# Kernel tuning notes

Measured on AMD Instinct MI355X. Metric: run time of the kernel, lower is better.

The kernel has to match this reference:

```python
import jax, jax.numpy as jnp
import numpy as np

B, C, W, H = 4, 256, 64, 64
DK = C // 8  # query/key channels


def setup_inputs() -> dict:
    key = jax.random.key(0)
    ks = jax.random.split(key, 7)
    x = jax.random.normal(ks[0], (B, C, W, H), dtype=jnp.float32)
    # conv1x1 weights stored as [out_ch, in_ch]
    Wq = jax.random.normal(ks[1], (DK, C), dtype=jnp.float32) / np.sqrt(C)
    bq = jnp.zeros((DK,), dtype=jnp.float32)
    Wk = jax.random.normal(ks[2], (DK, C), dtype=jnp.float32) / np.sqrt(C)
    bk = jnp.zeros((DK,), dtype=jnp.float32)
    Wv = jax.random.normal(ks[3], (C, C), dtype=jnp.float32) / np.sqrt(C)
    bv = jnp.zeros((C,), dtype=jnp.float32)
    gamma = jnp.zeros((1,), dtype=jnp.float32)
    return {"x": x, "Wq": Wq, "bq": bq, "Wk": Wk, "bk": bk,
            "Wv": Wv, "bv": bv, "gamma": gamma}


def reference(x, Wq, bq, Wk, bk, Wv, bv, gamma):
    b, c, w, h = x.shape
    n = w * h
    xf = x.reshape(b, c, n)                     # [B, C, N]
    # conv1x1 == channel matmul
    q = jnp.einsum('dc,bcn->bnd', Wq, xf) + bq  # [B, N, DK]
    k = jnp.einsum('dc,bcn->bdn', Wk, xf) + bk[None, :, None]  # [B, DK, N]
    energy = jnp.einsum('bnd,bdm->bnm', q, k)   # [B, N, N]
    attention = jax.nn.softmax(energy, axis=-1)
    v = jnp.einsum('dc,bcn->bdn', Wv, xf) + bv[None, :, None]  # [B, C, N]
    out = jnp.einsum('bdm,bnm->bdn', v, attention)              # [B, C, N]
    out = out.reshape(b, c, w, h)
    out = gamma * out + x
    return out, attention
```

## Files before the change

### kernel.cpp

```cpp
#include <hip/hip_runtime.h>
#include <hip/hip_bf16.h>

typedef __attribute__((ext_vector_type(8))) short bf16x8;
typedef __attribute__((ext_vector_type(4))) float f32x4;
typedef __attribute__((ext_vector_type(4))) unsigned int u32x4;
typedef __attribute__((ext_vector_type(2))) unsigned int u32x2;

#define B_SZ 4
#define C_SZ 256
#define N_SZ 4096
#define DK_SZ 32

#define WQB_OFF 0
#define WKB_OFF 8192
#define WVB_OFF 16384
#define QB_OFF  81920
#define KB_OFF  606208
#define VB_OFF  1130496

__device__ __forceinline__ short f2bf(float f) {
    union { float f; unsigned int u; } v; v.f = f;
    unsigned int r = v.u + 0x7fffu + ((v.u >> 16) & 1u);
    return (short)(r >> 16);
}

__device__ __forceinline__ unsigned int cvt_pk_bf16(float lo, float hi) {
    unsigned int r;
    asm volatile("v_cvt_pk_bf16_f32 %0, %1, %2" : "=v"(r) : "v"(lo), "v"(hi));
    return r;
}

__device__ __forceinline__ f32x4 mfma16(bf16x8 a, bf16x8 b, f32x4 c) {
    return __builtin_amdgcn_mfma_f32_16x16x32_bf16(a, b, c, 0, 0, 0);
}

__device__ __forceinline__ void gload_lds16(const void* g, void* l) {
    __builtin_amdgcn_global_load_lds((const __attribute__((address_space(1))) unsigned int*)g,
                                     (__attribute__((address_space(3))) unsigned int*)l, 16, 0, 0);
}

__device__ __forceinline__ void remap_block(int i, int& b, int& n0) {
    b = (i & 7) >> 1;
    n0 = (((i >> 3) << 1) | (i & 1)) * 64;
}

__global__ __launch_bounds__(256) void k_convw(const float* __restrict__ Wq,
                                               const float* __restrict__ Wk,
                                               const float* __restrict__ Wv,
                                               short* __restrict__ ws) {
    int i = blockIdx.x * 256 + threadIdx.x;
    if (i < 8192) {
        ws[WQB_OFF + i] = f2bf(Wq[i]);
        ws[WKB_OFF + i] = f2bf(Wk[i]);
    }
    ws[WVB_OFF + i] = f2bf(Wv[i]);
}

__global__ __launch_bounds__(256) void k_prep(const float* __restrict__ x,
                                              const float* __restrict__ bq,
                                              const float* __restrict__ bk,
                                              const float* __restrict__ bv,
                                              short* __restrict__ ws) {
    __shared__ short xsT[64][264];
    __shared__ short vt_s[64][258];

    int b, n0;
    remap_block(blockIdx.x, b, n0);
    const int t = threadIdx.x;
    const float* xb = x + (size_t)b * C_SZ * N_SZ;

    {
        int c0 = t >> 4, n4 = (t & 15) * 4;
#pragma unroll
        for (int i = 0; i < 16; i++) {
            int c = c0 + 16 * i;
            float4 v = *(const float4*)(xb + (size_t)c * N_SZ + n0 + n4);
            xsT[n4 + 0][c] = f2bf(v.x);
            xsT[n4 + 1][c] = f2bf(v.y);
            xsT[n4 + 2][c] = f2bf(v.z);
            xsT[n4 + 3][c] = f2bf(v.w);
        }
    }
    __syncthreads();

    const int w = t >> 6, l = t & 63;
    const int lr = l & 15, lk = l >> 4;

    bf16x8 af[8];
#pragma unroll
    for (int kk = 0; kk < 8; kk++)
        af[kk] = *(const bf16x8*)(&xsT[w * 16 + lr][kk * 32 + lk * 8]);

#pragma unroll
    for (int qk = 0; qk < 2; qk++) {
        const short* wb = ws + (qk ? WKB_OFF : WQB_OFF);
        const float* bias = qk ? bk : bq;
        short* outp = ws + (qk ? KB_OFF : QB_OFF) + (size_t)b * N_SZ * DK_SZ;
#pragma unroll
        for (int cf = 0; cf < 2; cf++) {
            f32x4 acc = {0.f, 0.f, 0.f, 0.f};
#pragma unroll
            for (int kk = 0; kk < 8; kk++) {
                bf16x8 bfr = *(const bf16x8*)(wb + (cf * 16 + lr) * 256 + kk * 32 + lk * 8);
                acc = mfma16(af[kk], bfr, acc);
            }
            float bias_v = bias[cf * 16 + lr];
#pragma unroll
            for (int r = 0; r < 4; r++) {
                int row = w * 16 + lk * 4 + r;
                outp[(size_t)(n0 + row) * DK_SZ + cf * 16 + lr] = f2bf(acc[r] + bias_v);
            }
        }
    }

#pragma unroll
    for (int cf = 0; cf < 16; cf++) {
        f32x4 acc = {0.f, 0.f, 0.f, 0.f};
#pragma unroll
        for (int kk = 0; kk < 8; kk++) {
            bf16x8 bfr = *(const bf16x8*)(ws + WVB_OFF + (cf * 16 + lr) * 256 + kk * 32 + lk * 8);
            acc = mfma16(af[kk], bfr, acc);
        }
        float bias_v = bv[cf * 16 + lr];
#pragma unroll
        for (int r = 0; r < 4; r++) {
            vt_s[w * 16 + lk * 4 + r][cf * 16 + lr] = f2bf(acc[r] + bias_v);
        }
    }
    __syncthreads();
    {
        short* vb = ws + VB_OFF + (size_t)b * C_SZ * N_SZ;
        int nn = t & 63;
#pragma unroll
        for (int i = 0; i < 64; i++) {
            int c = (t >> 6) + 4 * i;
            vb[(size_t)c * N_SZ + n0 + nn] = vt_s[nn][c];
        }
    }
}

__global__ __launch_bounds__(512, 1) void k_attn(const short* __restrict__ ws,
                                                 const float* __restrict__ x,
                                                 const float* __restrict__ gamma_p,
                                                 float* __restrict__ out) {
    __shared__ short v_lds[3][16384];
    __shared__ short k_lds[3][2304];
    __shared__ short p_lds[2][64][72];
    __shared__ float rsum_s[2][64];

    int b, n0;
    remap_block(blockIdx.x, b, n0);
    const int t = threadIdx.x, w = t >> 6, l = t & 63;
    const int rg = w & 3, ch = w >> 2;
    const int lr = l & 15, lk = l >> 4;

    const short* qb = ws + QB_OFF + (size_t)b * N_SZ * DK_SZ;
    const short* kb = ws + KB_OFF + (size_t)b * N_SZ * DK_SZ;
    const short* vb = ws + VB_OFF + (size_t)b * C_SZ * N_SZ;
    const char* kbb = (const char*)kb;

    bf16x8 qf = *(const bf16x8*)(qb + (size_t)(n0 + rg * 16 + lr) * DK_SZ + lk * 8);

    float rs = 0.f;
    for (int mt = 0; mt < 32; mt++) {
        int mb = ch * 2048 + mt * 64;
        bf16x8 kfa = *(const bf16x8*)(kb + (size_t)(mb + lr) * DK_SZ + lk * 8);
        bf16x8 kfb = *(const bf16x8*)(kb + (size_t)(mb + 16 + lr) * DK_SZ + lk * 8);
        bf16x8 kfc = *(const bf16x8*)(kb + (size_t)(mb + 32 + lr) * DK_SZ + lk * 8);
        bf16x8 kfd = *(const bf16x8*)(kb + (size_t)(mb + 48 + lr) * DK_SZ + lk * 8);
        f32x4 s0 = mfma16(kfa, qf, (f32x4){0.f, 0.f, 0.f, 0.f});
        f32x4 s1 = mfma16(kfb, qf, (f32x4){0.f, 0.f, 0.f, 0.f});
        f32x4 s2 = mfma16(kfc, qf, (f32x4){0.f, 0.f, 0.f, 0.f});
        f32x4 s3 = mfma16(kfd, qf, (f32x4){0.f, 0.f, 0.f, 0.f});
#pragma unroll
        for (int r = 0; r < 4; r++)
            rs += __expf(s0[r]) + __expf(s1[r]) + __expf(s2[r]) + __expf(s3[r]);
    }
    rs += __shfl_xor(rs, 16);
    rs += __shfl_xor(rs, 32);
    if (l < 16) rsum_s[ch][rg * 16 + l] = rs;
    __syncthreads();
    const float invp = 1.f / (rsum_s[0][rg * 16 + lr] + rsum_s[1][rg * 16 + lr]);

    float* attn_row = out + (size_t)B_SZ * C_SZ * N_SZ + (size_t)b * N_SZ * N_SZ
                      + (size_t)(n0 + rg * 16 + lr) * N_SZ;
    f32x4 O[4][4];
#pragma unroll
    for (int cf = 0; cf < 4; cf++)
#pragma unroll
        for (int rgi = 0; rgi < 4; rgi++) O[cf][rgi] = (f32x4){0.f, 0.f, 0.f, 0.f};

    const int krow = ch * 32 + lr;
    const int kswz = ((lk ^ ((lr >> 1) & 3)) << 4);
    const int aoff = rg * 8192 + lr * 128 + ((((ch << 2) + lk) ^ (lr & 7)) << 4);
    const int boff = lr * 144 + ch * 64 + lk * 16;

    bf16x8 kf0, kf1;

#define STAGE(tt, buf)                                                              \
    {                                                                               \
        const int krw = w * 8 + (l >> 2);                                           \
        const int ksl = (l & 3) ^ ((l >> 3) & 3);                                   \
        gload_lds16(kbb + (size_t)(tt) * 4096 + krw * 64 + ksl * 16,                \
                    (void*)&k_lds[buf][w * 256]);                                   \
        const int mb = (tt) * 64;                                                   \
        _Pragma("unroll")                                                           \
        for (int i = 0; i < 4; i++) {                                               \
            int c = w * 32 + i * 8 + (l >> 3);                                      \
            int j = l & 7;                                                          \
            const short* gp = vb + (size_t)c * N_SZ + mb + ((j ^ (c & 7)) << 3);    \
            gload_lds16(gp, (void*)&v_lds[buf][(w * 32 + i * 8) * 64]);             \
        }                                                                           \
    }

#define KREAD(tt)                                                                   \
    {                                                                               \
        const char* kl = (const char*)&k_lds[(tt) % 3][0];                          \
        kf0 = *(const bf16x8*)(kl + krow * 64 + kswz);                              \
        kf1 = *(const bf16x8*)(kl + krow * 64 + 1024 + kswz);                       \
    }

#define SCOMP_BODY(tt, pb)                                                          \
    {                                                                               \
        f32x4 s0 = mfma16(kf0, qf, (f32x4){0.f, 0.f, 0.f, 0.f});                    \
        f32x4 s1 = mfma16(kf1, qf, (f32x4){0.f, 0.f, 0.f, 0.f});                    \
        f32x4 ev0, ev1;                                                             \
        ev0[0] = __expf(s0[0]) * invp; ev0[1] = __expf(s0[1]) * invp;               \
        ev0[2] = __expf(s0[2]) * invp; ev0[3] = __expf(s0[3]) * invp;               \
        ev1[0] = __expf(s1[0]) * invp; ev1[1] = __expf(s1[1]) * invp;               \
        ev1[2] = __expf(s1[2]) * invp; ev1[3] = __expf(s1[3]) * invp;               \
        const int mbase = (tt) * 64 + ch * 32 + 4 * lk;                             \
        __builtin_nontemporal_store(ev0, (f32x4*)(attn_row + mbase));               \
        __builtin_nontemporal_store(ev1, (f32x4*)(attn_row + mbase + 16));          \
        u32x2 pk0, pk1;                                                             \
        pk0[0] = cvt_pk_bf16(ev0[0], ev0[1]); pk0[1] = cvt_pk_bf16(ev0[2], ev0[3]); \
        pk1[0] = cvt_pk_bf16(ev1[0], ev1[1]); pk1[1] = cvt_pk_bf16(ev1[2], ev1[3]); \
        *(u32x2*)(&p_lds[pb][rg * 16 + lr][ch * 32 + lk * 4]) = pk0;                \
        *(u32x2*)(&p_lds[pb][rg * 16 + lr][ch * 32 + 16 + lk * 4]) = pk1;           \
    }

    STAGE(0, 0);
    STAGE(1, 1);
    __builtin_amdgcn_sched_barrier(0);
    asm volatile("s_waitcnt vmcnt(5)" ::: "memory");
    __builtin_amdgcn_sched_barrier(0);
    __builtin_amdgcn_s_barrier();
    KREAD(0);
    SCOMP_BODY(0, 0);

    for (int mt = 0; mt < 64; mt++) {
        asm volatile("s_waitcnt vmcnt(2) lgkmcnt(0)" ::: "memory");
        __builtin_amdgcn_sched_barrier(0);
        __builtin_amdgcn_s_barrier();
        __builtin_amdgcn_sched_barrier(0);
        const int cur = mt & 1;
        if (mt < 63) KREAD(mt + 1);
        if (mt < 62) STAGE(mt + 2, (mt + 2) % 3);
        __builtin_amdgcn_sched_barrier(0);
        if (mt < 63) SCOMP_BODY(mt + 1, cur ^ 1);
        __builtin_amdgcn_sched_barrier(0);
        const char* vbase = (const char*)&v_lds[mt % 3][0];
        const char* pbase = (const char*)&p_lds[cur][0][0];
        bf16x8 Afr[4], Bfr[4];
#pragma unroll
        for (int cf = 0; cf < 4; cf++)
            Afr[cf] = *(const bf16x8*)(vbase + cf * 2048 + aoff);
#pragma unroll
        for (int rgi = 0; rgi < 4; rgi++)
            Bfr[rgi] = *(const bf16x8*)(pbase + rgi * 2304 + boff);
#pragma unroll
        for (int cf = 0; cf < 4; cf++)
#pragma unroll
            for (int rgi = 0; rgi < 4; rgi++)
                O[cf][rgi] = mfma16(Afr[cf], Bfr[rgi], O[cf][rgi]);
    }
#undef STAGE
#undef KREAD
#undef SCOMP_BODY

    __syncthreads();
    float* o_red = (float*)&v_lds[0][0];
    const int RSTRIDE = 4360;
    if (ch == 1) {
#pragma unroll
        for (int cf = 0; cf < 4; cf++)
#pragma unroll
            for (int rgi = 0; rgi < 4; rgi++)
#pragma unroll
                for (int r = 0; r < 4; r++)
                    o_red[rgi * RSTRIDE + (rg * 64 + cf * 16 + 4 * lk + r) * 17 + lr] = O[cf][rgi][r];
    }
    __syncthreads();
    if (ch == 0) {
#pragma unroll
        for (int cf = 0; cf < 4; cf++)
#pragma unroll
            for (int rgi = 0; rgi < 4; rgi++)
#pragma unroll
                for (int r = 0; r < 4; r++) {
                    int idx = rgi * RSTRIDE + (rg * 64 + cf * 16 + 4 * lk + r) * 17 + lr;
                    o_red[idx] += O[cf][rgi][r];
                }
    }
    __syncthreads();
    {
        const float g = gamma_p[0];
        const float* xb = x + (size_t)b * C_SZ * N_SZ;
        float* ob = out + (size_t)b * C_SZ * N_SZ;
        int nn = t & 63;
        int c0 = t >> 6;
        int rbase = (nn >> 4) * RSTRIDE + (nn & 15);
#pragma unroll
        for (int i = 0; i < 32; i++) {
            int c = c0 + 8 * i;
            size_t idx = (size_t)c * N_SZ + n0 + nn;
            ob[idx] = g * o_red[rbase + c * 17] + xb[idx];
        }
    }
}

extern "C" void kernel_launch(void* const* d_in, const int* in_sizes, int n_in,
                              void* d_out, int out_size, void* d_ws, size_t ws_size,
                              hipStream_t stream) {
    const float* x     = (const float*)d_in[0];
    const float* Wq    = (const float*)d_in[1];
    const float* bq    = (const float*)d_in[2];
    const float* Wk    = (const float*)d_in[3];
    const float* bk    = (const float*)d_in[4];
    const float* Wv    = (const float*)d_in[5];
    const float* bv    = (const float*)d_in[6];
    const float* gamma = (const float*)d_in[7];
    short* ws = (short*)d_ws;
    float* out = (float*)d_out;

    hipLaunchKernelGGL(k_convw, dim3(256), dim3(256), 0, stream, Wq, Wk, Wv, ws);
    hipLaunchKernelGGL(k_prep, dim3(256), dim3(256), 0, stream, x, bq, bk, bv, ws);
    hipLaunchKernelGGL(k_attn, dim3(256), dim3(512), 0, stream, ws, x, gamma, out);
}
```

Before: 137.3 us.

## Replace LDS-staged barrier pipeline with per-wave private P tiles and direct global loads

The attention kernel drops the triple-buffered global-to-LDS staging of K and V and the per-iteration block barriers. Each wave now computes the whole 64x64 probability tile for its key chunk into a private LDS area, then reads V fragments straight from global memory for the PV MFMAs. Attention-matrix stores are rewritten so each wave stores its 16 rows as 16-byte vectors read back from LDS. This removes block-wide synchronisation, but the QK^T and exp work is now repeated in four waves, and the stored attention values are bf16-rounded instead of fp32, which costs accuracy.

```diff
diff --git a/kernel.cpp b/kernel.cpp
--- a/kernel.cpp
+++ b/kernel.cpp
@@ -24,6 +24,11 @@
     return (short)(r >> 16);
 }
 
+__device__ __forceinline__ float asf(unsigned int u) {
+    union { unsigned int u; float f; } v; v.u = u;
+    return v.f;
+}
+
 __device__ __forceinline__ unsigned int cvt_pk_bf16(float lo, float hi) {
     unsigned int r;
     asm volatile("v_cvt_pk_bf16_f32 %0, %1, %2" : "=v"(r) : "v"(lo), "v"(hi));
@@ -32,11 +37,6 @@
 
 __device__ __forceinline__ f32x4 mfma16(bf16x8 a, bf16x8 b, f32x4 c) {
     return __builtin_amdgcn_mfma_f32_16x16x32_bf16(a, b, c, 0, 0, 0);
-}
-
-__device__ __forceinline__ void gload_lds16(const void* g, void* l) {
-    __builtin_amdgcn_global_load_lds((const __attribute__((address_space(1))) unsigned int*)g,
-                                     (__attribute__((address_space(3))) unsigned int*)l, 16, 0, 0);
 }
 
 __device__ __forceinline__ void remap_block(int i, int& b, int& n0) {
@@ -143,162 +143,131 @@
                                                  const float* __restrict__ x,
                                                  const float* __restrict__ gamma_p,
                                                  float* __restrict__ out) {
-    __shared__ short v_lds[3][16384];
-    __shared__ short k_lds[3][2304];
-    __shared__ short p_lds[2][64][72];
+    __shared__ short p_all[8][4608];
     __shared__ float rsum_s[2][64];
 
     int b, n0;
     remap_block(blockIdx.x, b, n0);
     const int t = threadIdx.x, w = t >> 6, l = t & 63;
-    const int rg = w & 3, ch = w >> 2;
+    const int cq = w & 3, mh = w >> 2;
     const int lr = l & 15, lk = l >> 4;
 
     const short* qb = ws + QB_OFF + (size_t)b * N_SZ * DK_SZ;
     const short* kb = ws + KB_OFF + (size_t)b * N_SZ * DK_SZ;
     const short* vb = ws + VB_OFF + (size_t)b * C_SZ * N_SZ;
-    const char* kbb = (const char*)kb;
-
-    bf16x8 qf = *(const bf16x8*)(qb + (size_t)(n0 + rg * 16 + lr) * DK_SZ + lk * 8);
-
-    float rs = 0.f;
-    for (int mt = 0; mt < 32; mt++) {
-        int mb = ch * 2048 + mt * 64;
-        bf16x8 kfa = *(const bf16x8*)(kb + (size_t)(mb + lr) * DK_SZ + lk * 8);
-        bf16x8 kfb = *(const bf16x8*)(kb + (size_t)(mb + 16 + lr) * DK_SZ + lk * 8);
-        bf16x8 kfc = *(const bf16x8*)(kb + (size_t)(mb + 32 + lr) * DK_SZ + lk * 8);
-        bf16x8 kfd = *(const bf16x8*)(kb + (size_t)(mb + 48 + lr) * DK_SZ + lk * 8);
-        f32x4 s0 = mfma16(kfa, qf, (f32x4){0.f, 0.f, 0.f, 0.f});
-        f32x4 s1 = mfma16(kfb, qf, (f32x4){0.f, 0.f, 0.f, 0.f});
-        f32x4 s2 = mfma16(kfc, qf, (f32x4){0.f, 0.f, 0.f, 0.f});
-        f32x4 s3 = mfma16(kfd, qf, (f32x4){0.f, 0.f, 0.f, 0.f});
-#pragma unroll
-        for (int r = 0; r < 4; r++)
-            rs += __expf(s0[r]) + __expf(s1[r]) + __expf(s2[r]) + __expf(s3[r]);
-    }
-    rs += __shfl_xor(rs, 16);
-    rs += __shfl_xor(rs, 32);
-    if (l < 16) rsum_s[ch][rg * 16 + l] = rs;
-    __syncthreads();
-    const float invp = 1.f / (rsum_s[0][rg * 16 + lr] + rsum_s[1][rg * 16 + lr]);
-
-    float* attn_row = out + (size_t)B_SZ * C_SZ * N_SZ + (size_t)b * N_SZ * N_SZ
-                      + (size_t)(n0 + rg * 16 + lr) * N_SZ;
+
+    {
+        bf16x8 qf1 = *(const bf16x8*)(qb + (size_t)(n0 + cq * 16 + lr) * DK_SZ + lk * 8);
+        float rs = 0.f;
+        for (int mt = 0; mt < 32; mt++) {
+            int mb = mh * 2048 + mt * 64;
+            bf16x8 kfa = *(const bf16x8*)(kb + (size_t)(mb + lr) * DK_SZ + lk * 8);
+            bf16x8 kfb = *(const bf16x8*)(kb + (size_t)(mb + 16 + lr) * DK_SZ + lk * 8);
+            bf16x8 kfc = *(const bf16x8*)(kb + (size_t)(mb + 32 + lr) * DK_SZ + lk * 8);
+            bf16x8 kfd = *(const bf16x8*)(kb + (size_t)(mb + 48 + lr) * DK_SZ + lk * 8);
+            f32x4 s0 = mfma16(kfa, qf1, (f32x4){0.f, 0.f, 0.f, 0.f});
+            f32x4 s1 = mfma16(kfb, qf1, (f32x4){0.f, 0.f, 0.f, 0.f});
+            f32x4 s2 = mfma16(kfc, qf1, (f32x4){0.f, 0.f, 0.f, 0.f});
+            f32x4 s3 = mfma16(kfd, qf1, (f32x4){0.f, 0.f, 0.f, 0.f});
+#pragma unroll
+            for (int r = 0; r < 4; r++)
+                rs += __expf(s0[r]) + __expf(s1[r]) + __expf(s2[r]) + __expf(s3[r]);
+        }
+        rs += __shfl_xor(rs, 16);
+        rs += __shfl_xor(rs, 32);
+        if (l < 16) rsum_s[mh][cq * 16 + l] = rs;
+    }
+    __syncthreads();
+    float invp4[4];
+#pragma unroll
+    for (int rg = 0; rg < 4; rg++)
+        invp4[rg] = 1.f / (rsum_s[0][rg * 16 + lr] + rsum_s[1][rg * 16 + lr]);
+
+    bf16x8 qfr[4];
+#pragma unroll
+    for (int rg = 0; rg < 4; rg++)
+        qfr[rg] = *(const bf16x8*)(qb + (size_t)(n0 + rg * 16 + lr) * DK_SZ + lk * 8);
+
+    float* attn_b = out + (size_t)B_SZ * C_SZ * N_SZ + (size_t)b * N_SZ * N_SZ;
+    short* pw = &p_all[w][0];
     f32x4 O[4][4];
 #pragma unroll
     for (int cf = 0; cf < 4; cf++)
 #pragma unroll
         for (int rgi = 0; rgi < 4; rgi++) O[cf][rgi] = (f32x4){0.f, 0.f, 0.f, 0.f};
 
-    const int krow = ch * 32 + lr;
-    const int kswz = ((lk ^ ((lr >> 1) & 3)) << 4);
-    const int aoff = rg * 8192 + lr * 128 + ((((ch << 2) + lk) ^ (lr & 7)) << 4);
-    const int boff = lr * 144 + ch * 64 + lk * 16;
-
-    bf16x8 kf0, kf1;
-
-#define STAGE(tt, buf)                                                              \
-    {                                                                               \
-        const int krw = w * 8 + (l >> 2);                                           \
-        const int ksl = (l & 3) ^ ((l >> 3) & 3);                                   \
-        gload_lds16(kbb + (size_t)(tt) * 4096 + krw * 64 + ksl * 16,                \
-                    (void*)&k_lds[buf][w * 256]);                                   \
-        const int mb = (tt) * 64;                                                   \
-        _Pragma("unroll")                                                           \
-        for (int i = 0; i < 4; i++) {                                               \
-            int c = w * 32 + i * 8 + (l >> 3);                                      \
-            int j = l & 7;                                                          \
-            const short* gp = vb + (size_t)c * N_SZ + mb + ((j ^ (c & 7)) << 3);    \
-            gload_lds16(gp, (void*)&v_lds[buf][(w * 32 + i * 8) * 64]);             \
-        }                                                                           \
-    }
-
-#define KREAD(tt)                                                                   \
-    {                                                                               \
-        const char* kl = (const char*)&k_lds[(tt) % 3][0];                          \
-        kf0 = *(const bf16x8*)(kl + krow * 64 + kswz);                              \
-        kf1 = *(const bf16x8*)(kl + krow * 64 + 1024 + kswz);                       \
-    }
-
-#define SCOMP_BODY(tt, pb)                                                          \
-    {                                                                               \
-        f32x4 s0 = mfma16(kf0, qf, (f32x4){0.f, 0.f, 0.f, 0.f});                    \
-        f32x4 s1 = mfma16(kf1, qf, (f32x4){0.f, 0.f, 0.f, 0.f});                    \
-        f32x4 ev0, ev1;                                                             \
-        ev0[0] = __expf(s0[0]) * invp; ev0[1] = __expf(s0[1]) * invp;               \
-        ev0[2] = __expf(s0[2]) * invp; ev0[3] = __expf(s0[3]) * invp;               \
-        ev1[0] = __expf(s1[0]) * invp; ev1[1] = __expf(s1[1]) * invp;               \
-        ev1[2] = __expf(s1[2]) * invp; ev1[3] = __expf(s1[3]) * invp;               \
-        const int mbase = (tt) * 64 + ch * 32 + 4 * lk;                             \
-        __builtin_nontemporal_store(ev0, (f32x4*)(attn_row + mbase));               \
-        __builtin_nontemporal_store(ev1, (f32x4*)(attn_row + mbase + 16));          \
-        u32x2 pk0, pk1;                                                             \
-        pk0[0] = cvt_pk_bf16(ev0[0], ev0[1]); pk0[1] = cvt_pk_bf16(ev0[2], ev0[3]); \
-        pk1[0] = cvt_pk_bf16(ev1[0], ev1[1]); pk1[1] = cvt_pk_bf16(ev1[2], ev1[3]); \
-        *(u32x2*)(&p_lds[pb][rg * 16 + lr][ch * 32 + lk * 4]) = pk0;                \
-        *(u32x2*)(&p_lds[pb][rg * 16 + lr][ch * 32 + 16 + lk * 4]) = pk1;           \
-    }
-
-    STAGE(0, 0);
-    STAGE(1, 1);
-    __builtin_amdgcn_sched_barrier(0);
-    asm volatile("s_waitcnt vmcnt(5)" ::: "memory");
-    __builtin_amdgcn_sched_barrier(0);
-    __builtin_amdgcn_s_barrier();
-    KREAD(0);
-    SCOMP_BODY(0, 0);
-
-    for (int mt = 0; mt < 64; mt++) {
-        asm volatile("s_waitcnt vmcnt(2) lgkmcnt(0)" ::: "memory");
-        __builtin_amdgcn_sched_barrier(0);
-        __builtin_amdgcn_s_barrier();
-        __builtin_amdgcn_sched_barrier(0);
-        const int cur = mt & 1;
-        if (mt < 63) KREAD(mt + 1);
-        if (mt < 62) STAGE(mt + 2, (mt + 2) % 3);
-        __builtin_amdgcn_sched_barrier(0);
-        if (mt < 63) SCOMP_BODY(mt + 1, cur ^ 1);
-        __builtin_amdgcn_sched_barrier(0);
-        const char* vbase = (const char*)&v_lds[mt % 3][0];
-        const char* pbase = (const char*)&p_lds[cur][0][0];
-        bf16x8 Afr[4], Bfr[4];
+    for (int mc = 0; mc < 32; mc++) {
+        const int m0 = mh * 2048 + mc * 64;
+
+#pragma unroll
+        for (int mf = 0; mf < 4; mf++) {
+            bf16x8 kf = *(const bf16x8*)(kb + (size_t)(m0 + mf * 16 + lr) * DK_SZ + lk * 8);
+#pragma unroll
+            for (int rg = 0; rg < 4; rg++) {
+                f32x4 s = mfma16(kf, qfr[rg], (f32x4){0.f, 0.f, 0.f, 0.f});
+                const float iv = invp4[rg];
+                u32x2 pk;
+                pk[0] = cvt_pk_bf16(__expf(s[0]) * iv, __expf(s[1]) * iv);
+                pk[1] = cvt_pk_bf16(__expf(s[2]) * iv, __expf(s[3]) * iv);
+                const int row = rg * 16 + lr;
+                const int j = 2 * mf + (lk >> 1);
+                *(u32x2*)(pw + row * 72 + (((j + row) & 7) << 3) + 4 * (lk & 1)) = pk;
+            }
+        }
+
+#pragma unroll
+        for (int i = 0; i < 4; i++) {
+            const int row = cq * 16 + i * 4 + (l >> 4);
+            const int c4 = l & 15;
+            const int j = c4 >> 1;
+            u32x2 u = *(const u32x2*)(pw + row * 72 + (((j + row) & 7) << 3) + 4 * (c4 & 1));
+            f32x4 f;
+            f[0] = asf(u[0] << 16); f[1] = asf(u[0] & 0xffff0000u);
+            f[2] = asf(u[1] << 16); f[3] = asf(u[1] & 0xffff0000u);
+            __builtin_nontemporal_store(f, (f32x4*)(attn_b + (size_t)(n0 + row) * N_SZ + m0 + c4 * 4));
+        }
+
+#pragma unroll
+        for (int k2 = 0; k2 < 2; k2++) {
+            bf16x8 Bf[4], Af[4];
+#pragma unroll
+            for (int rgi = 0; rgi < 4; rgi++) {
+                const int row = rgi * 16 + lr;
+                const int j = 4 * k2 + lk;
+                Bf[rgi] = *(const bf16x8*)(pw + row * 72 + (((j + row) & 7) << 3));
+            }
+#pragma unroll
+            for (int cf = 0; cf < 4; cf++)
+                Af[cf] = *(const bf16x8*)(vb + (size_t)(cq * 64 + cf * 16 + lr) * N_SZ + m0 + k2 * 32 + lk * 8);
+#pragma unroll
+            for (int cf = 0; cf < 4; cf++)
+#pragma unroll
+                for (int rgi = 0; rgi < 4; rgi++)
+                    O[cf][rgi] = mfma16(Af[cf], Bf[rgi], O[cf][rgi]);
+        }
+    }
+
+    __syncthreads();
+    float* o_red = (float*)&p_all[0][0];
+    const int RSTRIDE = 4360;
+    if (mh == 1) {
 #pragma unroll
         for (int cf = 0; cf < 4; cf++)
-            Afr[cf] = *(const bf16x8*)(vbase + cf * 2048 + aoff);
-#pragma unroll
-        for (int rgi = 0; rgi < 4; rgi++)
-            Bfr[rgi] = *(const bf16x8*)(pbase + rgi * 2304 + boff);
+#pragma unroll
+            for (int rgi = 0; rgi < 4; rgi++)
+#pragma unroll
+                for (int r = 0; r < 4; r++)
+                    o_red[rgi * RSTRIDE + (cq * 64 + cf * 16 + 4 * lk + r) * 17 + lr] = O[cf][rgi][r];
+    }
+    __syncthreads();
+    if (mh == 0) {
 #pragma unroll
         for (int cf = 0; cf < 4; cf++)
 #pragma unroll
             for (int rgi = 0; rgi < 4; rgi++)
-                O[cf][rgi] = mfma16(Afr[cf], Bfr[rgi], O[cf][rgi]);
-    }
-#undef STAGE
-#undef KREAD
-#undef SCOMP_BODY
-
-    __syncthreads();
-    float* o_red = (float*)&v_lds[0][0];
-    const int RSTRIDE = 4360;
-    if (ch == 1) {
-#pragma unroll
-        for (int cf = 0; cf < 4; cf++)
-#pragma unroll
-            for (int rgi = 0; rgi < 4; rgi++)
-#pragma unroll
-                for (int r = 0; r < 4; r++)
-                    o_red[rgi * RSTRIDE + (rg * 64 + cf * 16 + 4 * lk + r) * 17 + lr] = O[cf][rgi][r];
-    }
-    __syncthreads();
-    if (ch == 0) {
-#pragma unroll
-        for (int cf = 0; cf < 4; cf++)
-#pragma unroll
-            for (int rgi = 0; rgi < 4; rgi++)
 #pragma unroll
                 for (int r = 0; r < 4; r++) {
-                    int idx = rgi * RSTRIDE + (rg * 64 + cf * 16 + 4 * lk + r) * 17 + lr;
+                    int idx = rgi * RSTRIDE + (cq * 64 + cf * 16 + 4 * lk + r) * 17 + lr;
                     o_red[idx] += O[cf][rgi][r];
                 }
     }
```

Result: slower. 192.0 us (+39.8%).
